# Optimization experiments

Measured on AMD Instinct MI355X. Metric: run time of the kernel, lower is better.

The kernel has to match this reference:

```python
import jax, jax.numpy as jnp
import numpy as np

N_VOCAB_TOTAL = 32064  # n_vocab + n_nts
D_MODEL = 256


def setup_inputs() -> dict:
    key = jax.random.key(0)
    ks = jax.random.split(key, 8)
    d = D_MODEL
    tokens = jax.random.randint(ks[0], (64, 4095), 0, N_VOCAB_TOTAL, dtype=jnp.int32)
    # embedding_tgt: normal with std 1/sqrt(d) (reset_parameters)
    E = jax.random.normal(ks[1], (N_VOCAB_TOTAL, d), dtype=jnp.float32) / jnp.sqrt(jnp.float32(d))
    s_in = 1.0 / np.sqrt(3 * d)
    s_h = 1.0 / np.sqrt(d)
    W_in = jax.random.uniform(ks[2], (d, 3 * d), jnp.float32, -s_in, s_in)  # Linear(3d, d)
    b_in = jax.random.uniform(ks[3], (d,), jnp.float32, -s_in, s_in)
    W1 = jax.random.uniform(ks[4], (d, d), jnp.float32, -s_h, s_h)
    b1 = jax.random.uniform(ks[5], (d,), jnp.float32, -s_h, s_h)
    W2 = jax.random.uniform(ks[6], (d, d), jnp.float32, -s_h, s_h)
    b2 = jax.random.uniform(ks[7], (d,), jnp.float32, -s_h, s_h)
    return {"tokens": tokens, "E": E, "W_in": W_in, "b_in": b_in,
            "W1": W1, "b1": b1, "W2": W2, "b2": b2}


def _bin_agg(roots, left, right, W_in, b_in, W1, b1, W2, b2):
    # skipmlp_binary_agg: root + hidden(inp(cat([root,left,right])))
    # hidden = ELU -> Linear -> ELU -> Linear  (nlayers=2)
    x = jnp.concatenate([roots, left, right], axis=-1)        # [..., 3d]
    h = x @ W_in.T + b_in                                     # inp: Linear(3d, d)
    h = jax.nn.elu(h) @ W1.T + b1
    h = jax.nn.elu(h) @ W2.T + b2
    return roots + h


def reference(tokens, E, W_in, b_in, W1, b1, W2, b2):
    # tokens: [B, N] heap-ordered perfect binary trees, N = 2^(D+1)-1.
    B, N = tokens.shape
    n_leaves = (N + 1) // 2
    emb = E[tokens]                                           # [B, N, d] gather
    cur = emb[:, N - n_leaves:]                               # leaf level, [B, 2^D, d]
    level = n_leaves // 2
    while level >= 1:                                          # fixed D iterations
        roots = emb[:, level - 1: 2 * level - 1]               # [B, level, d]
        left = cur[:, 0::2]
        right = cur[:, 1::2]
        cur = _bin_agg(roots, left, right, W_in, b_in, W1, b1, W2, b2)
        level //= 2
    return cur[:, 0]                                           # [B, d] root embeddings
```

## Files before the change

### kernel.cpp

```cpp
#include <hip/hip_runtime.h>
#include <stdint.h>


typedef __attribute__((ext_vector_type(8))) short short8;
typedef __attribute__((ext_vector_type(4))) float f32x4;

typedef const __attribute__((address_space(1))) unsigned int* gas_ptr;
typedef __attribute__((address_space(3))) unsigned int* las_ptr;

#define TOK_N 4095

__device__ __forceinline__ unsigned short f32_to_bf16(float f) {
    union { float f; unsigned u; } v; v.f = f;
    return (unsigned short)((v.u + 0x7fffu + ((v.u >> 16) & 1u)) >> 16);
}
__device__ __forceinline__ float bf16_to_f32(unsigned short u) {
    union { unsigned u; float f; } v; v.u = ((unsigned)u) << 16; return v.f;
}

__global__ void convert_f32_bf16(const float* __restrict__ E,
                                 const float* __restrict__ Win,
                                 const float* __restrict__ W1,
                                 const float* __restrict__ W2,
                                 unsigned short* __restrict__ Ebf,
                                 unsigned short* __restrict__ Winbf,
                                 unsigned short* __restrict__ W1bf,
                                 unsigned short* __restrict__ W2bf) {
    const int nE = 32064 * 256, nWin = 256 * 768, nW = 256 * 256;
    const int total4 = (nE + nWin + 2 * nW) >> 2;
    for (int i = blockIdx.x * blockDim.x + threadIdx.x; i < total4;
         i += gridDim.x * blockDim.x) {
        int idx = i << 2;
        const float* src; unsigned short* dst; int off;
        if (idx < nE)                  { src = E;   dst = Ebf;   off = idx; }
        else if (idx < nE + nWin)      { src = Win; dst = Winbf; off = idx - nE; }
        else if (idx < nE + nWin + nW) { src = W1;  dst = W1bf;  off = idx - nE - nWin; }
        else                           { src = W2;  dst = W2bf;  off = idx - nE - nWin - nW; }
        float4 f = *(const float4*)(src + off);
        ushort4 o;
        o.x = f32_to_bf16(f.x); o.y = f32_to_bf16(f.y);
        o.z = f32_to_bf16(f.z); o.w = f32_to_bf16(f.w);
        *(ushort4*)(dst + off) = o;
    }
}

template<int MT, int DEPTH, int WROW>
__device__ __forceinline__ void run_pass(const unsigned short* __restrict__ Xs,
                                         const unsigned short* __restrict__ wlane,
                                         int kbase, f32x4 (&acc)[MT][4],
                                         int l15, int q)
{
    const int xm = l15 & 7;
    short8 bb[DEPTH][4];
#pragma unroll
    for (int d = 0; d < DEPTH; ++d)
#pragma unroll
        for (int nt = 0; nt < 4; ++nt)
            bb[d][nt] = *(const short8*)(wlane + (size_t)(nt * 16) * WROW + kbase + d * 32);
#pragma unroll
    for (int k = 0; k < 8; ++k) {
        short8 a[MT];
        const int sl = (((4 * k + q) ^ xm) << 3);
#pragma unroll
        for (int mt = 0; mt < MT; ++mt)
            a[mt] = *(const short8*)(Xs + (mt * 16 + l15) * 256 + sl);
#pragma unroll
        for (int mt = 0; mt < MT; ++mt)
#pragma unroll
            for (int nt = 0; nt < 4; ++nt)
                acc[mt][nt] = __builtin_amdgcn_mfma_f32_16x16x32_bf16(
                    a[mt], bb[k % DEPTH][nt], acc[mt][nt], 0, 0, 0);
        if (k + DEPTH < 8) {
#pragma unroll
            for (int nt = 0; nt < 4; ++nt)
                bb[k % DEPTH][nt] = *(const short8*)(wlane + (size_t)(nt * 16) * WROW + kbase + (k + DEPTH) * 32);
        }
    }
}

template<int MT, int LAST>
__global__ __launch_bounds__(256, 3)
void tree_level(const int* __restrict__ tokens,
                const unsigned short* __restrict__ Ebf,
                const unsigned short* __restrict__ Win,
                const unsigned short* __restrict__ W1,
                const unsigned short* __restrict__ W2,
                const float* __restrict__ b_in,
                const float* __restrict__ b1,
                const float* __restrict__ b2,
                const unsigned short* __restrict__ cur_in,
                unsigned short* __restrict__ cur_out,
                float* __restrict__ final_out,
                int L, int logL, int first)
{
    constexpr int R = MT * 16;
    constexpr int DEPTH = (MT >= 4) ? 2 : 4;
    __shared__ unsigned short Xs[R * 256];

    const int tid  = threadIdx.x;
    const int lane = tid & 63;
    const int wid  = tid >> 6;
    const int l15  = lane & 15;
    const int q    = lane >> 4;
    const int n0   = wid * 64;
    const int blk  = blockIdx.x;

    auto gather = [&](int p) {
#pragma unroll
        for (int t = 0; t < R / 8; ++t) {
            const int base_r = wid * (R / 4) + t * 2;
            const int r = base_r + (lane >> 5);
            const unsigned short* src;
            {
                int g = blk * R + r;
                int b = g >> logL;
                int i = g - (b << logL);
                if (p == 0) {
                    int tok = tokens[b * TOK_N + (L - 1) + i];
                    src = Ebf + (size_t)tok * 256;
                } else if (first) {
                    int tok = tokens[b * TOK_N + 2047 + 2 * i + (p - 1)];
                    src = Ebf + (size_t)tok * 256;
                } else {
                    src = cur_in + ((size_t)b * (2 * L) + 2 * i + (p - 1)) * 256;
                }
            }
            const int c = (lane & 31) ^ (r & 7);
            __builtin_amdgcn_global_load_lds(
                (gas_ptr)(const void*)(src + c * 8),
                (las_ptr)(void*)(Xs + base_r * 256), 16, 0, 0);
        }
    };

    f32x4 acc[MT][4];
    float bv[4];
    auto init_acc = [&](const float* __restrict__ bias) {
#pragma unroll
        for (int nt = 0; nt < 4; ++nt) bv[nt] = bias[n0 + nt * 16 + l15];
#pragma unroll
        for (int mt = 0; mt < MT; ++mt)
#pragma unroll
            for (int nt = 0; nt < 4; ++nt)
                acc[mt][nt] = (f32x4){bv[nt], bv[nt], bv[nt], bv[nt]};
    };
    auto store_elu = [&]() {
#pragma unroll
        for (int mt = 0; mt < MT; ++mt)
#pragma unroll
            for (int nt = 0; nt < 4; ++nt)
#pragma unroll
                for (int rr = 0; rr < 4; ++rr) {
                    int row = mt * 16 + q * 4 + rr;
                    int col = n0 + nt * 16 + l15;
                    float h = acc[mt][nt][rr];
                    h = h > 0.f ? h : (__expf(h) - 1.f);
                    int slot = (col >> 3) ^ (row & 7);
                    Xs[row * 256 + slot * 8 + (col & 7)] = f32_to_bf16(h);
                }
    };

    gather(0);
    __syncthreads();
    init_acc(b_in);
    const unsigned short* winlane = Win + q * 8 + (size_t)(n0 + l15) * 768;
    for (int p = 0; p < 3; ++p) {
        run_pass<MT, DEPTH, 768>(Xs, winlane, p * 256, acc, l15, q);
        __syncthreads();
        if (p < 2) {
            gather(p + 1);
            __syncthreads();
        }
    }
    store_elu();
    __syncthreads();

    init_acc(b1);
    run_pass<MT, DEPTH, 256>(Xs, W1 + q * 8 + (size_t)(n0 + l15) * 256, 0, acc, l15, q);
    __syncthreads();
    store_elu();
    __syncthreads();

    init_acc(b2);
    run_pass<MT, DEPTH, 256>(Xs, W2 + q * 8 + (size_t)(n0 + l15) * 256, 0, acc, l15, q);
    __syncthreads();

    gather(0);
    __syncthreads();

    if (LAST) {
#pragma unroll
        for (int mt = 0; mt < MT; ++mt)
#pragma unroll
            for (int nt = 0; nt < 4; ++nt)
#pragma unroll
                for (int rr = 0; rr < 4; ++rr) {
                    int row = mt * 16 + q * 4 + rr;
                    int col = n0 + nt * 16 + l15;
                    int slot = (col >> 3) ^ (row & 7);
                    float o = acc[mt][nt][rr] +
                              bf16_to_f32(Xs[row * 256 + slot * 8 + (col & 7)]);
                    final_out[(size_t)(blk * R + row) * 256 + col] = o;
                }
    } else {
#pragma unroll
        for (int mt = 0; mt < MT; ++mt)
#pragma unroll
            for (int nt = 0; nt < 4; ++nt)
#pragma unroll
                for (int rr = 0; rr < 4; ++rr) {
                    int row = mt * 16 + q * 4 + rr;
                    int col = n0 + nt * 16 + l15;
                    int slot = (col >> 3) ^ (row & 7);
                    int a = row * 256 + slot * 8 + (col & 7);
                    float o = acc[mt][nt][rr] + bf16_to_f32(Xs[a]);
                    Xs[a] = f32_to_bf16(o);
                }
        __syncthreads();
        const int s  = tid & 31;
        const int sub = tid >> 5;
#pragma unroll
        for (int it = 0; it < R / 8; ++it) {
            int r = it * 8 + sub;
            int c = s ^ (r & 7);
            *(short8*)(cur_out + (size_t)(blk * R + r) * 256 + c * 8) =
                *(const short8*)(Xs + r * 256 + s * 8);
        }
    }
}

template<int MT, int LAST>
static void launch_level(const int* tokens, const unsigned short* Ebf,
                         const unsigned short* Win, const unsigned short* W1,
                         const unsigned short* W2, const float* b_in,
                         const float* b1, const float* b2,
                         const unsigned short* cin, unsigned short* cout,
                         float* out, int L, int first, hipStream_t stream) {
    int logL = 31 - __builtin_clz((unsigned)L);
    int blocks = (64 * L) / (16 * MT);
    tree_level<MT, LAST><<<dim3(blocks), dim3(256), 0, stream>>>(
        tokens, Ebf, Win, W1, W2, b_in, b1, b2, cin, cout, out, L, logL, first);
}

extern "C" void kernel_launch(void* const* d_in, const int* in_sizes, int n_in,
                              void* d_out, int out_size, void* d_ws, size_t ws_size,
                              hipStream_t stream) {
    const int*   tokens = (const int*)  d_in[0];
    const float* E      = (const float*)d_in[1];
    const float* W_in   = (const float*)d_in[2];
    const float* b_in   = (const float*)d_in[3];
    const float* W1     = (const float*)d_in[4];
    const float* b1     = (const float*)d_in[5];
    const float* W2     = (const float*)d_in[6];
    const float* b2     = (const float*)d_in[7];
    float* out = (float*)d_out;
    char* ws = (char*)d_ws;

    unsigned short* Ebf   = (unsigned short*)(ws);
    unsigned short* Winbf = (unsigned short*)(ws + 16416768);
    unsigned short* W1bf  = (unsigned short*)(ws + 16809984);
    unsigned short* W2bf  = (unsigned short*)(ws + 16941056);
    unsigned short* curA  = (unsigned short*)(ws + 17072128);
    unsigned short* curB  = (unsigned short*)(ws + 50626560);

    convert_f32_bf16<<<1024, 256, 0, stream>>>(E, W_in, W1, W2,
                                               Ebf, Winbf, W1bf, W2bf);

    const unsigned short* cin = curB;
    unsigned short* cout = curA;
    int first = 1;
    for (int L = 1024; L >= 1; L >>= 1) {
        int last = (L == 1);
        if (L >= 512)
            launch_level<4, 0>(tokens, Ebf, Winbf, W1bf, W2bf, b_in, b1, b2,
                               cin, cout, nullptr, L, first, stream);
        else if (L >= 128)
            launch_level<2, 0>(tokens, Ebf, Winbf, W1bf, W2bf, b_in, b1, b2,
                               cin, cout, nullptr, L, first, stream);
        else if (!last)
            launch_level<1, 0>(tokens, Ebf, Winbf, W1bf, W2bf, b_in, b1, b2,
                               cin, cout, nullptr, L, first, stream);
        else
            launch_level<1, 1>(tokens, Ebf, Winbf, W1bf, W2bf, b_in, b1, b2,
                               cin, cout, out, L, first, stream);
        cin = cout;
        cout = (cout == curA) ? curB : curA;
        first = 0;
    }
}
```

Measured before the change: 542.1 us.

## Overlap left/right child gathers with first input-projection pass using separate LDS buffers

Adds two more LDS buffers so the gathers for the left and right children are issued midway through the root-part MFMA pass instead of serialized between passes. The root embedding stays resident in Xs for the residual add, which removes the final re-gather. Weight prefetch is restructured so the last two K-slices are loaded up front. Levels 512 and up now use MT=2 instead of MT=4 to keep LDS and register use in check. This triples LDS per block, which may reduce occupancy, and means more, smaller blocks at the big levels.

```diff
diff --git a/kernel.cpp b/kernel.cpp
--- a/kernel.cpp
+++ b/kernel.cpp
@@ -44,21 +44,31 @@
     }
 }
 
-template<int MT, int DEPTH, int WROW>
+template<int MT, int WROW, typename F>
 __device__ __forceinline__ void run_pass(const unsigned short* __restrict__ Xs,
                                          const unsigned short* __restrict__ wlane,
                                          int kbase, f32x4 (&acc)[MT][4],
-                                         int l15, int q)
+                                         int l15, int q, F&& late)
 {
     const int xm = l15 & 7;
-    short8 bb[DEPTH][4];
-#pragma unroll
-    for (int d = 0; d < DEPTH; ++d)
+    short8 bb[2][4], bt[2][4];
+#pragma unroll
+    for (int d = 0; d < 2; ++d)
 #pragma unroll
         for (int nt = 0; nt < 4; ++nt)
             bb[d][nt] = *(const short8*)(wlane + (size_t)(nt * 16) * WROW + kbase + d * 32);
 #pragma unroll
+    for (int d = 0; d < 2; ++d)
+#pragma unroll
+        for (int nt = 0; nt < 4; ++nt)
+            bt[d][nt] = *(const short8*)(wlane + (size_t)(nt * 16) * WROW + kbase + (6 + d) * 32);
+#pragma unroll
     for (int k = 0; k < 8; ++k) {
+        if (k == 4) {
+            __builtin_amdgcn_sched_barrier(0);
+            late();
+            __builtin_amdgcn_sched_barrier(0);
+        }
         short8 a[MT];
         const int sl = (((4 * k + q) ^ xm) << 3);
 #pragma unroll
@@ -69,11 +79,12 @@
 #pragma unroll
             for (int nt = 0; nt < 4; ++nt)
                 acc[mt][nt] = __builtin_amdgcn_mfma_f32_16x16x32_bf16(
-                    a[mt], bb[k % DEPTH][nt], acc[mt][nt], 0, 0, 0);
-        if (k + DEPTH < 8) {
-#pragma unroll
-            for (int nt = 0; nt < 4; ++nt)
-                bb[k % DEPTH][nt] = *(const short8*)(wlane + (size_t)(nt * 16) * WROW + kbase + (k + DEPTH) * 32);
+                    a[mt], (k >= 6) ? bt[k - 6][nt] : bb[k & 1][nt],
+                    acc[mt][nt], 0, 0, 0);
+        if (k < 4) {
+#pragma unroll
+            for (int nt = 0; nt < 4; ++nt)
+                bb[k & 1][nt] = *(const short8*)(wlane + (size_t)(nt * 16) * WROW + kbase + (k + 2) * 32);
         }
     }
 }
@@ -94,8 +105,9 @@
                 int L, int logL, int first)
 {
     constexpr int R = MT * 16;
-    constexpr int DEPTH = (MT >= 4) ? 2 : 4;
     __shared__ unsigned short Xs[R * 256];
+    __shared__ unsigned short Hs[R * 256];
+    __shared__ unsigned short Gs[R * 256];
 
     const int tid  = threadIdx.x;
     const int lane = tid & 63;
@@ -105,7 +117,7 @@
     const int n0   = wid * 64;
     const int blk  = blockIdx.x;
 
-    auto gather = [&](int p) {
+    auto gather = [&](int p, unsigned short* dst) {
 #pragma unroll
         for (int t = 0; t < R / 8; ++t) {
             const int base_r = wid * (R / 4) + t * 2;
@@ -128,22 +140,27 @@
             const int c = (lane & 31) ^ (r & 7);
             __builtin_amdgcn_global_load_lds(
                 (gas_ptr)(const void*)(src + c * 8),
-                (las_ptr)(void*)(Xs + base_r * 256), 16, 0, 0);
+                (las_ptr)(void*)(dst + base_r * 256), 16, 0, 0);
         }
     };
 
+    float bva[4], bvb[4], bvc[4];
+#pragma unroll
+    for (int nt = 0; nt < 4; ++nt) {
+        bva[nt] = b_in[n0 + nt * 16 + l15];
+        bvb[nt] = b1[n0 + nt * 16 + l15];
+        bvc[nt] = b2[n0 + nt * 16 + l15];
+    }
+
     f32x4 acc[MT][4];
-    float bv[4];
-    auto init_acc = [&](const float* __restrict__ bias) {
-#pragma unroll
-        for (int nt = 0; nt < 4; ++nt) bv[nt] = bias[n0 + nt * 16 + l15];
+    auto init_acc = [&](const float* bv) {
 #pragma unroll
         for (int mt = 0; mt < MT; ++mt)
 #pragma unroll
             for (int nt = 0; nt < 4; ++nt)
                 acc[mt][nt] = (f32x4){bv[nt], bv[nt], bv[nt], bv[nt]};
     };
-    auto store_elu = [&]() {
+    auto store_elu = [&](unsigned short* dst) {
 #pragma unroll
         for (int mt = 0; mt < MT; ++mt)
 #pragma unroll
@@ -155,37 +172,33 @@
                     float h = acc[mt][nt][rr];
                     h = h > 0.f ? h : (__expf(h) - 1.f);
                     int slot = (col >> 3) ^ (row & 7);
-                    Xs[row * 256 + slot * 8 + (col & 7)] = f32_to_bf16(h);
+                    dst[row * 256 + slot * 8 + (col & 7)] = f32_to_bf16(h);
                 }
     };
 
-    gather(0);
-    __syncthreads();
-    init_acc(b_in);
+    gather(0, Xs);
+    __syncthreads();
+    init_acc(bva);
     const unsigned short* winlane = Win + q * 8 + (size_t)(n0 + l15) * 768;
-    for (int p = 0; p < 3; ++p) {
-        run_pass<MT, DEPTH, 768>(Xs, winlane, p * 256, acc, l15, q);
-        __syncthreads();
-        if (p < 2) {
-            gather(p + 1);
-            __syncthreads();
-        }
-    }
-    store_elu();
-    __syncthreads();
-
-    init_acc(b1);
-    run_pass<MT, DEPTH, 256>(Xs, W1 + q * 8 + (size_t)(n0 + l15) * 256, 0, acc, l15, q);
-    __syncthreads();
-    store_elu();
-    __syncthreads();
-
-    init_acc(b2);
-    run_pass<MT, DEPTH, 256>(Xs, W2 + q * 8 + (size_t)(n0 + l15) * 256, 0, acc, l15, q);
-    __syncthreads();
-
-    gather(0);
-    __syncthreads();
+    run_pass<MT, 768>(Xs, winlane, 0, acc, l15, q, [&]() {
+        gather(1, Hs);
+        gather(2, Gs);
+    });
+    __syncthreads();
+    run_pass<MT, 768>(Hs, winlane, 256, acc, l15, q, []() {});
+    __syncthreads();
+    run_pass<MT, 768>(Gs, winlane, 512, acc, l15, q, []() {});
+    store_elu(Hs);
+    __syncthreads();
+
+    init_acc(bvb);
+    run_pass<MT, 256>(Hs, W1 + q * 8 + (size_t)(n0 + l15) * 256, 0, acc, l15, q, []() {});
+    __syncthreads();
+    store_elu(Hs);
+    __syncthreads();
+
+    init_acc(bvc);
+    run_pass<MT, 256>(Hs, W2 + q * 8 + (size_t)(n0 + l15) * 256, 0, acc, l15, q, []() {});
 
     if (LAST) {
 #pragma unroll
@@ -202,6 +215,7 @@
                     final_out[(size_t)(blk * R + row) * 256 + col] = o;
                 }
     } else {
+        __syncthreads();
 #pragma unroll
         for (int mt = 0; mt < MT; ++mt)
 #pragma unroll
@@ -211,19 +225,19 @@
                     int row = mt * 16 + q * 4 + rr;
                     int col = n0 + nt * 16 + l15;
                     int slot = (col >> 3) ^ (row & 7);
-                    int a = row * 256 + slot * 8 + (col & 7);
-                    float o = acc[mt][nt][rr] + bf16_to_f32(Xs[a]);
-                    Xs[a] = f32_to_bf16(o);
+                    float o = acc[mt][nt][rr] +
+                              bf16_to_f32(Xs[row * 256 + slot * 8 + (col & 7)]);
+                    Gs[row * 256 + slot * 8 + (col & 7)] = f32_to_bf16(o);
                 }
         __syncthreads();
-        const int s  = tid & 31;
+        const int s   = tid & 31;
         const int sub = tid >> 5;
 #pragma unroll
         for (int it = 0; it < R / 8; ++it) {
             int r = it * 8 + sub;
             int c = s ^ (r & 7);
             *(short8*)(cur_out + (size_t)(blk * R + r) * 256 + c * 8) =
-                *(const short8*)(Xs + r * 256 + s * 8);
+                *(const short8*)(Gs + r * 256 + s * 8);
         }
     }
 }
@@ -270,10 +284,7 @@
     int first = 1;
     for (int L = 1024; L >= 1; L >>= 1) {
         int last = (L == 1);
-        if (L >= 512)
-            launch_level<4, 0>(tokens, Ebf, Winbf, W1bf, W2bf, b_in, b1, b2,
-                               cin, cout, nullptr, L, first, stream);
-        else if (L >= 128)
+        if (L >= 256)
             launch_level<2, 0>(tokens, Ebf, Winbf, W1bf, W2bf, b_in, b1, b2,
                                cin, cout, nullptr, L, first, stream);
         else if (!last)
```

Result: slower. 567.0 us (+4.6%).
